# Optimization experiments

Hardware: AMD Instinct MI355X
Metric: run time of the kernel (lower is better)

The kernel has to match this reference:

```python
import jax, jax.numpy as jnp
import numpy as np

B, T, DIM = 8, 4096, 1024
HEADS = 16
WS = [10, 20]
SHIFTS = [5, 10]
DIM_IN = DIM // 2        # bottleneck_ratio=0.5
DIM_BR = DIM_IN // 2     # per-branch channels
H_BR = HEADS // 2        # per-branch heads
EPS = 1e-6


def setup_inputs() -> dict:
    key = jax.random.key(0)
    ks = jax.random.split(key, 12)
    w = lambda k, s: (jax.random.normal(k, s) * 0.02).astype(jnp.float32)
    z = lambda n: jnp.zeros((n,), jnp.float32)
    return {
        "x": jax.random.normal(ks[0], (B, T, DIM), jnp.float32),
        "down_w": w(ks[1], (DIM, DIM_IN)), "down_b": z(DIM_IN),
        "up_w": w(ks[2], (DIM_IN, DIM)), "up_b": z(DIM),
        "norm1_w": jnp.ones((DIM_IN,), jnp.float32),
        "norm2_w": jnp.ones((DIM,), jnp.float32),
        "qkv1_w": w(ks[3], (DIM_BR, 3 * DIM_BR)), "qkv1_b": z(3 * DIM_BR),
        "proj1_w": w(ks[4], (DIM_BR, DIM_BR)), "proj1_b": z(DIM_BR),
        "rpb1": w(ks[5], (2 * WS[0] - 1, H_BR)),
        "qkv2_w": w(ks[6], (DIM_BR, 3 * DIM_BR)), "qkv2_b": z(3 * DIM_BR),
        "proj2_w": w(ks[7], (DIM_BR, DIM_BR)), "proj2_b": z(DIM_BR),
        "rpb2": w(ks[8], (2 * WS[1] - 1, H_BR)),
        "ffn_w1": w(ks[9], (DIM, 2 * DIM)), "ffn_b1": z(2 * DIM),
        "ffn_w2": w(ks[10], (2 * DIM, DIM)), "ffn_b2": z(DIM),
    }


def rmsnorm(x, w):
    return x * jax.lax.rsqrt(jnp.mean(x * x, axis=-1, keepdims=True) + EPS) * w


def _branch(x, window, shift, qkv_w, qkv_b, pw, pb, rpb, heads):
    # x: [B, T, C]; shifted-window attention along T with relative position bias
    Bx, Tn, C = x.shape
    pad = (-Tn) % window
    xp = jnp.pad(x, ((0, 0), (0, pad), (0, 0)))
    Tp = Tn + pad
    nW = Tp // window
    hd = C // heads
    scale = hd ** -0.5

    if shift > 0:
        xp = jnp.roll(xp, -shift, axis=1)
        m = np.zeros(Tp, np.float32)
        m[Tp - window:Tp - shift] = 1.0
        m[Tp - shift:] = 2.0
        mw = m.reshape(nW, window)
        amask = jnp.asarray(np.where(mw[:, :, None] != mw[:, None, :], -100.0, 0.0).astype(np.float32))  # [nW,w,w]
    else:
        amask = None

    xw = xp.reshape(Bx, nW, window, C)
    qkv = (xw @ qkv_w + qkv_b).reshape(Bx, nW, window, 3, heads, hd)
    q, k, v = qkv[:, :, :, 0], qkv[:, :, :, 1], qkv[:, :, :, 2]  # [B,nW,w,h,hd]

    attn = jnp.einsum('bnqhd,bnkhd->bnhqk', q * scale, k)  # [B,nW,h,w,w]

    coords = np.arange(window)
    ridx = coords[:, None] - coords[None, :] + window - 1      # [w,w]
    bias = jnp.transpose(rpb[ridx], (2, 0, 1))                 # [h,w,w]
    attn = attn + bias[None, None]
    if amask is not None:
        attn = attn + amask[None, :, None]

    attn = jax.nn.softmax(attn, axis=-1)
    out = jnp.einsum('bnhqk,bnkhd->bnqhd', attn, v).reshape(Bx, nW, window, C)
    out = out @ pw + pb
    out = out.reshape(Bx, Tp, C)
    if shift > 0:
        out = jnp.roll(out, shift, axis=1)
    return out[:, :Tn]


def reference(x, down_w, down_b, up_w, up_b, norm1_w, norm2_w,
              qkv1_w, qkv1_b, proj1_w, proj1_b, rpb1,
              qkv2_w, qkv2_b, proj2_w, proj2_b, rpb2,
              ffn_w1, ffn_b1, ffn_w2, ffn_b2):
    residual = x
    xi = rmsnorm(x @ down_w + down_b, norm1_w)           # [B,T,DIM_IN]
    x1, x2 = xi[..., :DIM_BR], xi[..., DIM_BR:]
    o1 = _branch(x1, WS[0], SHIFTS[0], qkv1_w, qkv1_b, proj1_w, proj1_b, rpb1, H_BR)
    o2 = _branch(x2, WS[1], SHIFTS[1], qkv2_w, qkv2_b, proj2_w, proj2_b, rpb2, H_BR)
    xc = jnp.concatenate([o1, o2], axis=-1) @ up_w + up_b
    x = residual + xc
    h = rmsnorm(x, norm2_w)
    ffn = jax.nn.gelu(h @ ffn_w1 + ffn_b1, approximate=False) @ ffn_w2 + ffn_b2
    return x + ffn
```

## Files before the change

### kernel.cpp

```cpp
#include <hip/hip_runtime.h>
#include <hip/hip_bf16.h>
#include <math.h>

typedef __bf16 bf16x8_t __attribute__((ext_vector_type(8)));
typedef float f32x4_t __attribute__((ext_vector_type(4)));
typedef __hip_bfloat16 bf16;

__device__ __forceinline__ void gload_lds16(const bf16* gsrc, unsigned short* ldst) {
  __builtin_amdgcn_global_load_lds(
      (const __attribute__((address_space(1))) unsigned int*)gsrc,
      (__attribute__((address_space(3))) unsigned int*)ldst, 16, 0, 0);
}

__global__ __launch_bounds__(256) void f2b_kernel(const float* __restrict__ in,
                                                  bf16* __restrict__ out, size_t n) {
  size_t i = ((size_t)blockIdx.x * 256 + threadIdx.x) * 4;
  if (i + 4 <= n) {
    float4 v = *reinterpret_cast<const float4*>(in + i);
    union { bf16 b[4]; ushort4 u; } cv;
    cv.b[0] = __float2bfloat16(v.x);
    cv.b[1] = __float2bfloat16(v.y);
    cv.b[2] = __float2bfloat16(v.z);
    cv.b[3] = __float2bfloat16(v.w);
    *reinterpret_cast<ushort4*>(out + i) = cv.u;
  } else {
    for (; i < n; ++i) out[i] = __float2bfloat16(in[i]);
  }
}

__global__ __launch_bounds__(256) void transpose_f2b_kernel(const float* __restrict__ in,
                                                            bf16* __restrict__ out,
                                                            int K, int N) {
  __shared__ float t[32][33];
  int n0 = blockIdx.x * 32, k0 = blockIdx.y * 32;
  int tx = threadIdx.x & 31, ty = threadIdx.x >> 5;
#pragma unroll
  for (int i = 0; i < 32; i += 8)
    t[ty + i][tx] = in[(size_t)(k0 + ty + i) * N + n0 + tx];
  __syncthreads();
#pragma unroll
  for (int i = 0; i < 32; i += 8)
    out[(size_t)(n0 + ty + i) * K + k0 + tx] = __float2bfloat16(t[tx][ty + i]);
}

__global__ __launch_bounds__(256) void rmsnorm_kernel(const float* __restrict__ in,
                                                      const float* __restrict__ w,
                                                      bf16* __restrict__ out, int C) {
  int row = blockIdx.x;
  const float* r = in + (size_t)row * C;
  int tid = threadIdx.x;
  float ss = 0.f;
  for (int c = tid; c < C; c += 256) { float v = r[c]; ss += v * v; }
#pragma unroll
  for (int o = 32; o > 0; o >>= 1) ss += __shfl_down(ss, o, 64);
  __shared__ float part[4];
  if ((tid & 63) == 0) part[tid >> 6] = ss;
  __syncthreads();
  float inv = rsqrtf((part[0] + part[1] + part[2] + part[3]) / (float)C + 1e-6f);
  bf16* orow = out + (size_t)row * C;
  for (int c = tid; c < C; c += 256) orow[c] = __float2bfloat16(r[c] * inv * w[c]);
}

__global__ __launch_bounds__(256) void gather_kernel(const bf16* __restrict__ xi,
                                                     bf16* __restrict__ xb,
                                                     int Tp, int Tn, int shift, int coff) {
  size_t i = (size_t)blockIdx.x * 256 + threadIdx.x;
  int c = (int)(i & 255);
  size_t bt = i >> 8;
  int t = (int)(bt % (size_t)Tp);
  int b = (int)(bt / (size_t)Tp);
  int src = t + shift; if (src >= Tp) src -= Tp;
  bf16 v = __float2bfloat16(0.f);
  if (src < Tn) v = xi[(((size_t)b * Tn + src) << 9) + coff + c];
  xb[i] = v;
}

template <int W, int SHIFT>
__global__ void attn_kernel(const bf16* __restrict__ qkv, const float* __restrict__ rpb,
                            bf16* __restrict__ out, int nW, int Tp) {
  int blk = blockIdx.x;
  int b = blk / nW, n = blk % nW;
  int pair = threadIdx.x;
  if (pair >= 8 * W) return;
  int h = pair / W, qi = pair % W;
  size_t base = ((size_t)b * Tp + (size_t)n * W) * 768;
  float qv[32];
#pragma unroll
  for (int d = 0; d < 32; ++d) qv[d] = __bfloat162float(qkv[base + (size_t)qi * 768 + h * 32 + d]);
  const float scale = 0.17677669529663689f;
  float sc[W];
  float mx = -1e30f;
  for (int k = 0; k < W; ++k) {
    const bf16* kr = qkv + base + (size_t)k * 768 + 256 + h * 32;
    float dot = 0.f;
#pragma unroll
    for (int d = 0; d < 32; ++d) dot += qv[d] * __bfloat162float(kr[d]);
    float s = dot * scale + rpb[(qi - k + W - 1) * 8 + h];
    if (n == nW - 1) {
      bool lq = qi < (W - SHIFT), lk = k < (W - SHIFT);
      if (lq != lk) s -= 100.0f;
    }
    sc[k] = s;
    mx = fmaxf(mx, s);
  }
  float l = 0.f;
  for (int k = 0; k < W; ++k) { sc[k] = expf(sc[k] - mx); l += sc[k]; }
  float inv = 1.0f / l;
  float ov[32];
#pragma unroll
  for (int d = 0; d < 32; ++d) ov[d] = 0.f;
  for (int k = 0; k < W; ++k) {
    const bf16* vr = qkv + base + (size_t)k * 768 + 512 + h * 32;
    float p = sc[k];
#pragma unroll
    for (int d = 0; d < 32; ++d) ov[d] += p * __bfloat162float(vr[d]);
  }
  bf16* orow = out + ((size_t)b * Tp + (size_t)n * W + qi) * 256 + h * 32;
#pragma unroll
  for (int d = 0; d < 32; ++d) orow[d] = __float2bfloat16(ov[d] * inv);
}

template <int MODE>
__global__ __launch_bounds__(256) void gemm_kernel(
    const bf16* __restrict__ A, const bf16* __restrict__ Wt,
    const float* __restrict__ bias,
    float* outF, bf16* outB, const float* resid,
    int M, int N, int K, int ldc, int Tp, int Tn, int shift, int coff) {
  __shared__ unsigned short lA[128 * 32];
  __shared__ unsigned short lB[128 * 32];
  int tid = threadIdx.x;
  int wave = tid >> 6, lane = tid & 63;
  int m0 = blockIdx.y * 128, n0 = blockIdx.x * 128;
  int wm = (wave >> 1) * 64, wn = (wave & 1) * 64;
  int ml = lane & 15, koff = (lane >> 4) * 8;
  f32x4_t acc[4][4] = {};

  int lrow = lane >> 2;
  int lcol = (lane & 3) * 8;
  int ar0 = wave * 32;

  for (int k0 = 0; k0 < K; k0 += 32) {
    __syncthreads();
#pragma unroll
    for (int j = 0; j < 2; ++j) {
      int r = ar0 + j * 16;
      int gr = m0 + r + lrow; if (gr > M - 1) gr = M - 1;
      gload_lds16(A + (size_t)gr * K + k0 + lcol, &lA[r * 32]);
      int nr = n0 + r + lrow;
      gload_lds16(Wt + (size_t)nr * K + k0 + lcol, &lB[r * 32]);
    }
    __syncthreads();

    bf16x8_t fa[4], fb[4];
#pragma unroll
    for (int t = 0; t < 4; ++t) {
      fa[t] = *reinterpret_cast<const bf16x8_t*>(&lA[(wm + t * 16 + ml) * 32 + koff]);
      fb[t] = *reinterpret_cast<const bf16x8_t*>(&lB[(wn + t * 16 + ml) * 32 + koff]);
    }
#pragma unroll
    for (int mt = 0; mt < 4; ++mt)
#pragma unroll
      for (int nt = 0; nt < 4; ++nt)
        acc[mt][nt] = __builtin_amdgcn_mfma_f32_16x16x32_bf16(fa[mt], fb[nt], acc[mt][nt], 0, 0, 0);
  }

  int rbase = (lane >> 4) * 4;
#pragma unroll
  for (int mt = 0; mt < 4; ++mt)
#pragma unroll
    for (int nt = 0; nt < 4; ++nt)
#pragma unroll
      for (int i = 0; i < 4; ++i) {
        int row = m0 + wm + mt * 16 + rbase + i;
        int col = n0 + wn + nt * 16 + ml;
        if (row >= M) continue;
        float v = acc[mt][nt][i] + bias[col];
        if (MODE == 0) {
          outF[(size_t)row * ldc + col] = v;
        } else if (MODE == 1) {
          outB[(size_t)row * ldc + col] = __float2bfloat16(v);
        } else if (MODE == 2) {
          outF[(size_t)row * ldc + col] = v + resid[(size_t)row * ldc + col];
        } else if (MODE == 3) {
          v = 0.5f * v * (1.0f + erff(v * 0.70710678118654752f));
          outB[(size_t)row * ldc + col] = __float2bfloat16(v);
        } else if (MODE == 5) {
          int b = row / Tp;
          int t = row - b * Tp;
          int i2 = t + shift; if (i2 >= Tp) i2 -= Tp;
          if (i2 < Tn)
            outB[((size_t)b * Tn + i2) * ldc + coff + col] = __float2bfloat16(v);
        }
      }
}

extern "C" void kernel_launch(void* const* d_in, const int* in_sizes, int n_in,
                              void* d_out, int out_size, void* d_ws, size_t ws_size,
                              hipStream_t stream) {
  const float* x       = (const float*)d_in[0];
  const float* down_w  = (const float*)d_in[1];
  const float* down_b  = (const float*)d_in[2];
  const float* up_w    = (const float*)d_in[3];
  const float* up_b    = (const float*)d_in[4];
  const float* norm1_w = (const float*)d_in[5];
  const float* norm2_w = (const float*)d_in[6];
  const float* qkv1_w  = (const float*)d_in[7];
  const float* qkv1_b  = (const float*)d_in[8];
  const float* proj1_w = (const float*)d_in[9];
  const float* proj1_b = (const float*)d_in[10];
  const float* rpb1    = (const float*)d_in[11];
  const float* qkv2_w  = (const float*)d_in[12];
  const float* qkv2_b  = (const float*)d_in[13];
  const float* proj2_w = (const float*)d_in[14];
  const float* proj2_b = (const float*)d_in[15];
  const float* rpb2    = (const float*)d_in[16];
  const float* ffn_w1  = (const float*)d_in[17];
  const float* ffn_b1  = (const float*)d_in[18];
  const float* ffn_w2  = (const float*)d_in[19];
  const float* ffn_b2  = (const float*)d_in[20];
  float* out = (float*)d_out;

  const int Bb = 8, T = 4096, DIM = 1024, DIM_IN = 512;
  const int Tp = 4100, Tn = T;
  const int M  = Bb * T;
  const int Mp = Bb * Tp;
  const int nW1 = Tp / 10, nW2 = Tp / 20;

  char* ws = (char*)d_ws;
  const size_t MB = 1ull << 20;
  size_t wo = 0;
  auto walloc = [&](size_t elems) {
    bf16* p = (bf16*)(ws + wo);
    wo += ((elems * 2 + 255) & ~(size_t)255);
    return p;
  };
  bf16* w_down  = walloc(1024 * 512);
  bf16* w_up    = walloc(512 * 1024);
  bf16* w_qkv1  = walloc(256 * 768);
  bf16* w_proj1 = walloc(256 * 256);
  bf16* w_qkv2  = walloc(256 * 768);
  bf16* w_proj2 = walloc(256 * 256);
  bf16* w_ffn1  = walloc(1024 * 2048);
  bf16* w_ffn2  = walloc(2048 * 1024);
  bf16*  xbf     = (bf16*)(ws + 12 * MB);
  bf16*  xb1     = (bf16*)(ws + 12 * MB);
  bf16*  xb2     = (bf16*)(ws + 29 * MB);
  bf16*  att1    = (bf16*)(ws + 46 * MB);
  bf16*  att2    = (bf16*)(ws + 63 * MB);
  float* y1      = (float*)(ws + 80 * MB);
  bf16*  concatb = (bf16*)(ws + 80 * MB);
  bf16*  hbuf    = (bf16*)(ws + 80 * MB);
  bf16*  xi      = (bf16*)(ws + 144 * MB);
  bf16*  qkv1buf = (bf16*)(ws + 176 * MB);
  bf16*  qkv2buf = (bf16*)(ws + 225 * MB);
  bf16*  gbuf    = (bf16*)(ws + 144 * MB);

  auto cvt = [&](const float* src, bf16* dst, size_t n) {
    int grid = (int)((n / 4 + 255) / 256);
    hipLaunchKernelGGL(f2b_kernel, dim3(grid), dim3(256), 0, stream, src, dst, n);
  };
  auto tr = [&](const float* src, bf16* dst, int K, int N) {
    hipLaunchKernelGGL(transpose_f2b_kernel, dim3(N / 32, K / 32), dim3(256), 0, stream,
                       src, dst, K, N);
  };
  cvt(x, xbf, (size_t)M * DIM);
  tr(down_w, w_down, 1024, 512);
  tr(up_w, w_up, 512, 1024);
  tr(qkv1_w, w_qkv1, 256, 768);
  tr(proj1_w, w_proj1, 256, 256);
  tr(qkv2_w, w_qkv2, 256, 768);
  tr(proj2_w, w_proj2, 256, 256);
  tr(ffn_w1, w_ffn1, 1024, 2048);
  tr(ffn_w2, w_ffn2, 2048, 1024);

  auto gemm = [&](auto modeTag, const bf16* A, const bf16* Wt, const float* bias,
                  float* oF, bf16* oB, const float* res,
                  int Mm, int Nn, int Kk, int ldc, int tp, int tn, int sh, int co) {
    constexpr int MODE = decltype(modeTag)::value;
    hipLaunchKernelGGL((gemm_kernel<MODE>), dim3(Nn / 128, (Mm + 127) / 128), dim3(256), 0,
                       stream, A, Wt, bias, oF, oB, res, Mm, Nn, Kk, ldc, tp, tn, sh, co);
  };
  using I0 = std::integral_constant<int, 0>;
  using I1 = std::integral_constant<int, 1>;
  using I2 = std::integral_constant<int, 2>;
  using I3 = std::integral_constant<int, 3>;
  using I5 = std::integral_constant<int, 5>;

  gemm(I0{}, xbf, w_down, down_b, y1, nullptr, nullptr, M, DIM_IN, DIM, DIM_IN, 0, 0, 0, 0);
  hipLaunchKernelGGL(rmsnorm_kernel, dim3(M), dim3(256), 0, stream, y1, norm1_w, xi, DIM_IN);
  hipLaunchKernelGGL(gather_kernel, dim3(Mp), dim3(256), 0, stream, xi, xb1, Tp, Tn, 5, 0);
  hipLaunchKernelGGL(gather_kernel, dim3(Mp), dim3(256), 0, stream, xi, xb2, Tp, Tn, 10, 256);
  gemm(I1{}, xb1, w_qkv1, qkv1_b, nullptr, qkv1buf, nullptr, Mp, 768, 256, 768, 0, 0, 0, 0);
  gemm(I1{}, xb2, w_qkv2, qkv2_b, nullptr, qkv2buf, nullptr, Mp, 768, 256, 768, 0, 0, 0, 0);
  hipLaunchKernelGGL((attn_kernel<10, 5>), dim3(Bb * nW1), dim3(128), 0, stream,
                     qkv1buf, rpb1, att1, nW1, Tp);
  hipLaunchKernelGGL((attn_kernel<20, 10>), dim3(Bb * nW2), dim3(192), 0, stream,
                     qkv2buf, rpb2, att2, nW2, Tp);
  gemm(I5{}, att1, w_proj1, proj1_b, nullptr, concatb, nullptr, Mp, 256, 256, 512, Tp, Tn, 5, 0);
  gemm(I5{}, att2, w_proj2, proj2_b, nullptr, concatb, nullptr, Mp, 256, 256, 512, Tp, Tn, 10, 256);
  gemm(I2{}, concatb, w_up, up_b, out, nullptr, x, M, DIM, DIM_IN, DIM, 0, 0, 0, 0);
  hipLaunchKernelGGL(rmsnorm_kernel, dim3(M), dim3(256), 0, stream, out, norm2_w, hbuf, DIM);
  gemm(I3{}, hbuf, w_ffn1, ffn_b1, nullptr, gbuf, nullptr, M, 2048, DIM, 2048, 0, 0, 0, 0);
  gemm(I2{}, gbuf, w_ffn2, ffn_b2, out, nullptr, out, M, DIM, 2048, DIM, 0, 0, 0, 0);
  (void)in_sizes; (void)n_in; (void)out_size; (void)ws_size;
}
```

Measured before the change: 1.547 ms.

## Double-buffer GEMM LDS tiles and swizzle workgroups across XCDs

The GEMM kernel now keeps two LDS buffers per operand, so the global-to-LDS load of the next K-slice is issued before the MFMA compute on the current slice, with a single waitcnt+barrier per step in place of two syncthreads. It also remaps block IDs so that consecutive tiles land on the same XCD, aiming for better L2 reuse of A and B. The loop assumes K is a multiple of 64, and LDS use doubles, which may reduce occupancy.

```diff
diff --git a/kernel.cpp b/kernel.cpp
--- a/kernel.cpp
+++ b/kernel.cpp
@@ -10,6 +10,12 @@
   __builtin_amdgcn_global_load_lds(
       (const __attribute__((address_space(1))) unsigned int*)gsrc,
       (__attribute__((address_space(3))) unsigned int*)ldst, 16, 0, 0);
+}
+
+__device__ __forceinline__ void pipe_sync() {
+  asm volatile("s_waitcnt vmcnt(0)" ::: "memory");
+  __builtin_amdgcn_s_barrier();
+  asm volatile("" ::: "memory");
 }
 
 __global__ __launch_bounds__(256) void f2b_kernel(const float* __restrict__ in,
@@ -126,11 +132,22 @@
     const float* __restrict__ bias,
     float* outF, bf16* outB, const float* resid,
     int M, int N, int K, int ldc, int Tp, int Tn, int shift, int coff) {
-  __shared__ unsigned short lA[128 * 32];
-  __shared__ unsigned short lB[128 * 32];
+  __shared__ unsigned short lA0[128 * 32];
+  __shared__ unsigned short lB0[128 * 32];
+  __shared__ unsigned short lA1[128 * 32];
+  __shared__ unsigned short lB1[128 * 32];
   int tid = threadIdx.x;
   int wave = tid >> 6, lane = tid & 63;
-  int m0 = blockIdx.y * 128, n0 = blockIdx.x * 128;
+
+  int nx = gridDim.x;
+  int nwg = nx * gridDim.y;
+  int id = blockIdx.y * nx + blockIdx.x;
+  int q = nwg >> 3, r = nwg & 7;
+  int xcd = id & 7, pos = id >> 3;
+  int swz = (xcd < r ? xcd * (q + 1) : r * (q + 1) + (xcd - r) * q) + pos;
+  int bx = swz % nx, by = swz / nx;
+
+  int m0 = by * 128, n0 = bx * 128;
   int wm = (wave >> 1) * 64, wn = (wave & 1) * 64;
   int ml = lane & 15, koff = (lane >> 4) * 8;
   f32x4_t acc[4][4] = {};
@@ -139,29 +156,39 @@
   int lcol = (lane & 3) * 8;
   int ar0 = wave * 32;
 
-  for (int k0 = 0; k0 < K; k0 += 32) {
-    __syncthreads();
+  auto stage = [&](unsigned short* dA, unsigned short* dB, int k0) {
 #pragma unroll
     for (int j = 0; j < 2; ++j) {
-      int r = ar0 + j * 16;
-      int gr = m0 + r + lrow; if (gr > M - 1) gr = M - 1;
-      gload_lds16(A + (size_t)gr * K + k0 + lcol, &lA[r * 32]);
-      int nr = n0 + r + lrow;
-      gload_lds16(Wt + (size_t)nr * K + k0 + lcol, &lB[r * 32]);
+      int rr = ar0 + j * 16;
+      int gr = m0 + rr + lrow; if (gr > M - 1) gr = M - 1;
+      gload_lds16(A + (size_t)gr * K + k0 + lcol, &dA[rr * 32]);
+      int nr = n0 + rr + lrow;
+      gload_lds16(Wt + (size_t)nr * K + k0 + lcol, &dB[rr * 32]);
     }
-    __syncthreads();
-
+  };
+  auto compute = [&](const unsigned short* sA, const unsigned short* sB) {
     bf16x8_t fa[4], fb[4];
 #pragma unroll
     for (int t = 0; t < 4; ++t) {
-      fa[t] = *reinterpret_cast<const bf16x8_t*>(&lA[(wm + t * 16 + ml) * 32 + koff]);
-      fb[t] = *reinterpret_cast<const bf16x8_t*>(&lB[(wn + t * 16 + ml) * 32 + koff]);
+      fa[t] = *reinterpret_cast<const bf16x8_t*>(&sA[(wm + t * 16 + ml) * 32 + koff]);
+      fb[t] = *reinterpret_cast<const bf16x8_t*>(&sB[(wn + t * 16 + ml) * 32 + koff]);
     }
 #pragma unroll
     for (int mt = 0; mt < 4; ++mt)
 #pragma unroll
       for (int nt = 0; nt < 4; ++nt)
         acc[mt][nt] = __builtin_amdgcn_mfma_f32_16x16x32_bf16(fa[mt], fb[nt], acc[mt][nt], 0, 0, 0);
+  };
+
+  stage(lA0, lB0, 0);
+  pipe_sync();
+  for (int k0 = 0; k0 < K; k0 += 64) {
+    stage(lA1, lB1, k0 + 32);
+    compute(lA0, lB0);
+    pipe_sync();
+    if (k0 + 64 < K) stage(lA0, lB0, k0 + 64);
+    compute(lA1, lB1);
+    pipe_sync();
   }
 
   int rbase = (lane >> 4) * 4;
```

Result: faster. 1.490 ms (-3.6%).

## Triple-buffer GEMM LDS loads with swizzled layout and XCD-aware tile mapping

Applied to the files above, without the earlier changes.

Restructures the bf16 MFMA GEMM main loop into a three-stage LDS ring, prefetching K-tiles ahead and gating on vmcnt counts so global loads overlap compute. It also XOR-swizzles the 16-byte chunk placement in LDS to cut bank conflicts on fragment reads. Workgroup IDs are remapped so consecutive tiles land on the same XCD for L2 reuse, and MFMA issue is wrapped in s_setprio. LDS use triples, and the hand-written vmcnt values assume an exact number of outstanding loads per stage, which could reduce occupancy or be fragile.

```diff
diff --git a/kernel.cpp b/kernel.cpp
--- a/kernel.cpp
+++ b/kernel.cpp
@@ -126,42 +126,74 @@
     const float* __restrict__ bias,
     float* outF, bf16* outB, const float* resid,
     int M, int N, int K, int ldc, int Tp, int Tn, int shift, int coff) {
-  __shared__ unsigned short lA[128 * 32];
-  __shared__ unsigned short lB[128 * 32];
+  __shared__ unsigned short lA[3][128 * 32];
+  __shared__ unsigned short lB[3][128 * 32];
   int tid = threadIdx.x;
   int wave = tid >> 6, lane = tid & 63;
-  int m0 = blockIdx.y * 128, n0 = blockIdx.x * 128;
+
+  int nx = gridDim.x;
+  int nwg = nx * gridDim.y;
+  int id = blockIdx.y * nx + blockIdx.x;
+  int q = nwg >> 3, r = nwg & 7;
+  int xcd = id & 7, pos = id >> 3;
+  int swz = (xcd < r ? xcd * (q + 1) : r * (q + 1) + (xcd - r) * q) + pos;
+  int bx = swz % nx, by = swz / nx;
+
+  int m0 = by * 128, n0 = bx * 128;
   int wm = (wave >> 1) * 64, wn = (wave & 1) * 64;
-  int ml = lane & 15, koff = (lane >> 4) * 8;
+  int ml = lane & 15, cc = lane >> 4;
   f32x4_t acc[4][4] = {};
 
   int lrow = lane >> 2;
-  int lcol = (lane & 3) * 8;
-  int ar0 = wave * 32;
-
-  for (int k0 = 0; k0 < K; k0 += 32) {
-    __syncthreads();
+  int pchunk = lane & 3;
+
+  auto stage = [&](int buf, int k0) {
 #pragma unroll
     for (int j = 0; j < 2; ++j) {
-      int r = ar0 + j * 16;
-      int gr = m0 + r + lrow; if (gr > M - 1) gr = M - 1;
-      gload_lds16(A + (size_t)gr * K + k0 + lcol, &lA[r * 32]);
-      int nr = n0 + r + lrow;
-      gload_lds16(Wt + (size_t)nr * K + k0 + lcol, &lB[r * 32]);
+      int rr = wave * 32 + j * 16;
+      int row = rr + lrow;
+      int scol = (pchunk ^ ((row >> 1) & 3)) * 8;
+      int gr = m0 + row; if (gr > M - 1) gr = M - 1;
+      gload_lds16(A + (size_t)gr * K + k0 + scol, &lA[buf][rr * 32]);
+      int nr = n0 + row;
+      gload_lds16(Wt + (size_t)nr * K + k0 + scol, &lB[buf][rr * 32]);
     }
-    __syncthreads();
-
+  };
+  auto compute = [&](int buf) {
+    const unsigned short* sA = lA[buf];
+    const unsigned short* sB = lB[buf];
     bf16x8_t fa[4], fb[4];
 #pragma unroll
     for (int t = 0; t < 4; ++t) {
-      fa[t] = *reinterpret_cast<const bf16x8_t*>(&lA[(wm + t * 16 + ml) * 32 + koff]);
-      fb[t] = *reinterpret_cast<const bf16x8_t*>(&lB[(wn + t * 16 + ml) * 32 + koff]);
+      int ra = wm + t * 16 + ml;
+      fa[t] = *reinterpret_cast<const bf16x8_t*>(&sA[ra * 32 + ((cc ^ ((ra >> 1) & 3)) << 3)]);
+      int rb = wn + t * 16 + ml;
+      fb[t] = *reinterpret_cast<const bf16x8_t*>(&sB[rb * 32 + ((cc ^ ((rb >> 1) & 3)) << 3)]);
     }
+    __builtin_amdgcn_s_setprio(1);
 #pragma unroll
     for (int mt = 0; mt < 4; ++mt)
 #pragma unroll
       for (int nt = 0; nt < 4; ++nt)
         acc[mt][nt] = __builtin_amdgcn_mfma_f32_16x16x32_bf16(fa[mt], fb[nt], acc[mt][nt], 0, 0, 0);
+    __builtin_amdgcn_s_setprio(0);
+  };
+
+  int NT = K >> 5;
+  stage(0, 0);
+  stage(1, 32);
+  stage(2, 64);
+  int cur = 0;
+  for (int t = 0; t < NT; ++t) {
+    int rem = NT - 1 - t;
+    if (rem >= 2)      asm volatile("s_waitcnt vmcnt(8)" ::: "memory");
+    else if (rem == 1) asm volatile("s_waitcnt vmcnt(4)" ::: "memory");
+    else               asm volatile("s_waitcnt vmcnt(0)" ::: "memory");
+    __builtin_amdgcn_s_barrier();
+    compute(cur);
+    __builtin_amdgcn_s_barrier();
+    if (t + 3 < NT) stage(cur, (t + 3) * 32);
+    cur = cur + 1; if (cur == 3) cur = 0;
   }
 
   int rbase = (lane >> 4) * 4;
```

Result: no change. 1.542 ms (-0.3%).
